# Optimization experiments

Measured on AMD Instinct MI355X. Metric: run time of the kernel, lower is better.

Reference implementation:

```python
import jax, jax.numpy as jnp
import numpy as np
from jax import lax

N_STATES = 128
N_NL = 64
N_IN = 64
N_OUT = 32
N_SYS = 16
FILT = 24
GAMMA = 1e-3
Q_VAL = 10.0
BETA = 1e5
EPS = 1e-3
BATCH = 131072


def setup_inputs() -> dict:
    key = jax.random.key(0)
    ks = jax.random.split(key, 11)
    std = 0.1
    return {
        "inpt": jax.random.normal(ks[0], (BATCH, N_IN), jnp.float32),
        "state": jax.random.normal(ks[1], (BATCH, N_STATES), jnp.float32),
        "X": jax.random.normal(ks[2], (2 * N_STATES + N_NL, 2 * N_STATES + N_NL), jnp.float32) * std,
        "Y1": jax.random.normal(ks[3], (N_STATES, N_STATES), jnp.float32) * std,
        "X3": jax.random.normal(ks[4], (N_OUT, N_OUT), jnp.float32) * std,
        "Y3": jax.random.normal(ks[5], (N_OUT, N_OUT), jnp.float32) * std,
        "Z3": jax.random.normal(ks[6], (abs(N_IN - N_OUT), N_OUT), jnp.float32) * std,
        "B2": jax.random.normal(ks[7], (N_STATES, N_IN), jnp.float32) * std,
        "C2": jax.random.normal(ks[8], (N_OUT, N_STATES), jnp.float32) * std,
        "D21": jax.random.normal(ks[9], (N_OUT, N_NL), jnp.float32) * std,
        "D12": jax.random.normal(ks[10], (N_NL, N_IN), jnp.float32) * std,
    }


def _derived(X, Y1, X3, Y3, Z3, B2, C2, D21, D12):
    # set_model_param(): build contracting REN matrices from free params.
    s = min(N_IN, N_OUT)  # = N_OUT here
    Q = -Q_VAL * jnp.eye(N_OUT, dtype=X.dtype)
    m = N_IN - N_SYS
    R_diag = jnp.concatenate([
        BETA * jnp.ones(N_SYS), GAMMA * jnp.ones(FILT - 1),
        jnp.array([BETA]), GAMMA * jnp.ones(m - FILT)]).astype(X.dtype)
    R = jnp.diag(R_diag)
    I_s = jnp.eye(s, dtype=X.dtype)
    M = X3.T @ X3 + Y3 - Y3.T + Z3.T @ Z3 + EPS * I_s
    Minv = jnp.linalg.inv(I_s + M)
    # n_outputs < n_inputs branch
    N = jnp.concatenate([Minv @ (I_s - M), -2.0 * Minv @ Z3.T], axis=1)  # [n_out, n_in]
    Lq = jnp.linalg.cholesky(-Q).T
    Lr = jnp.linalg.cholesky(R).T
    D22 = jnp.linalg.inv(Lq) @ N @ Lr  # [n_out, n_in]
    R_cal = R + D22.T @ Q @ D22
    R_cal_inv = jnp.linalg.inv(R_cal)
    C2_cal = (D22.T @ Q @ C2).T            # [n_states, n_in]
    D21_cal = (D22.T @ Q @ D21).T - D12    # [n_nl, n_in]
    vec_r = jnp.concatenate([C2_cal, D21_cal, B2], axis=0)
    psi_r = vec_r @ R_cal_inv @ vec_r.T
    vec_q = jnp.concatenate([C2.T, D21.T, jnp.zeros((N_STATES, N_OUT), X.dtype)], axis=0)
    psi_q = vec_q @ Q @ vec_q.T
    n = 2 * N_STATES + N_NL
    H = X.T @ X + EPS * jnp.eye(n, dtype=X.dtype) + psi_r - psi_q
    ns, nl = N_STATES, N_NL
    H11 = H[:ns, :ns]
    H21 = H[ns:ns + nl, :ns]
    H22 = H[ns:ns + nl, ns:ns + nl]
    H31 = H[ns + nl:, :ns]
    H32 = H[ns + nl:, ns:ns + nl]
    H33 = H[ns + nl:, ns + nl:]
    Fm = H31
    B1 = H32
    E = 0.5 * (H11 + H33 + Y1 - Y1.T)
    Lam = 0.5 * jnp.diag(H22)
    D11 = -jnp.tril(H22, k=-1)  # strictly lower triangular
    C1 = -H21
    return Fm, B1, E, Lam, C1, D11, D22


def _ren_forward(inpt, state, X, Y1, X3, Y3, Z3, B2, C2, D21, D12):
    Fm, B1, E, Lam, C1, D11, D22 = _derived(X, Y1, X3, Y3, Z3, B2, C2, D21, D12)
    B = state.shape[0]
    # precompute the state/input contribution to every nonlinearity row
    a = state @ C1.T + inpt @ D12.T  # [B, n_nl] (bias = 0, bias=False)

    def step(w, xs):
        i, a_col, d11_row, lam = xs
        v = a_col + w @ d11_row                 # forward substitution: D11 strictly lower
        w = w.at[:, i].set(jnp.tanh(v / lam))
        return w, None

    w0 = jnp.zeros((B, N_NL), dtype=state.dtype)
    xs = (jnp.arange(N_NL), a.T, D11, Lam)
    w, _ = lax.scan(step, w0, xs)

    E_x_ = state @ Fm.T + w @ B1.T + inpt @ B2.T
    state_plus = E_x_ @ jnp.linalg.inv(E).T
    output = state @ C2.T + w @ D21.T + inpt @ D22.T
    return output, state_plus


def reference(inpt, state, X, Y1, X3, Y3, Z3, B2, C2, D21, D12):
    return _ren_forward(inpt, state, X, Y1, X3, Y3, Z3, B2, C2, D21, D12)
```

## Files before the change

### kernel.cpp

```cpp
#include <hip/hip_runtime.h>
#include <math.h>

#define BATCH 131072
#define NTOT 320

typedef __attribute__((ext_vector_type(8))) short short8;
typedef __attribute__((ext_vector_type(4))) float f32x4;

#define WS_D22   0
#define WS_VR    2048
#define WS_T     22528
#define WS_H     43008
#define WS_E     145408
#define WS_EINV  161792
#define WS_WEXT  178176
#define WS_D11   210944
#define WS_ILAM  215040
#define WS_BFU   215104
#define U_WATH 0
#define U_WATL 16384
#define U_WOT  32768
#define U_WSPH 40960
#define U_WSPL 73728
#define WS_M    (WS_H)
#define WS_A32M (WS_H + 1024)
#define WS_RC   (WS_H + 2048)
#define SC_AI   (WS_H)
#define SC_P    (WS_H + 4096)
#define SC_S    (WS_H + 8192)
#define SC_Q    (WS_H + 12288)
#define SC_R    (WS_H + 16384)

__device__ inline unsigned short f2bf(float x){
    unsigned u = __builtin_bit_cast(unsigned, x);
    u += 0x7FFFu + ((u >> 16) & 1u);
    return (unsigned short)(u >> 16);
}
__device__ inline float bf2f(unsigned short h){
    unsigned u = ((unsigned)h) << 16;
    return __builtin_bit_cast(float, u);
}
__device__ inline float r_diag(int j) {
    return (j < 16 || j == 39) ? 100000.0f : 0.001f;
}

__global__ __launch_bounds__(256) void k_der1a(
    const float* __restrict__ X3, const float* __restrict__ Y3,
    const float* __restrict__ Z3, float* __restrict__ ws)
{
    int idx = blockIdx.x*256 + threadIdx.x;
    if (idx >= 1024) return;
    int i = idx >> 5, j = idx & 31;
    float s = 0.f;
    for (int k = 0; k < 32; ++k)
        s += X3[k*32+i]*X3[k*32+j] + Z3[k*32+i]*Z3[k*32+j];
    s += Y3[i*32+j] - Y3[j*32+i];
    if (i == j) s += 0.001f;
    ws[WS_M + idx]    = s;
    ws[WS_A32M + idx] = s + (i == j ? 1.f : 0.f);
}

__global__ __launch_bounds__(1024) void k_gj32(float* __restrict__ ws)
{
    __shared__ float A32[32*33];
    const int t = threadIdx.x;
    const int i = t >> 5, j = t & 31;
    A32[i*33+j] = ws[WS_A32M + i*32 + j];
    __syncthreads();
    for (int k = 0; k < 32; ++k) {
        float ip = 1.f / A32[k*33+k];
        float f  = A32[i*33+k];
        float pj = A32[k*33+j];
        __syncthreads();
        float nv;
        if (i == k) nv = (j == k) ? ip : pj*ip;
        else        nv = (j == k) ? (-f*ip) : (A32[i*33+j] - f*ip*pj);
        A32[i*33+j] = nv;
        __syncthreads();
    }
    ws[WS_A32M + i*32 + j] = A32[i*33+j];
}

__global__ __launch_bounds__(512) void k_der1b(
    const float* __restrict__ Z3, float* __restrict__ ws)
{
    __shared__ float Ms[1024], Mi[1024], D22s[2048];
    const int t = threadIdx.x;
    for (int idx = t; idx < 1024; idx += 512) {
        Ms[idx] = ws[WS_M + idx];
        Mi[idx] = ws[WS_A32M + idx];
    }
    __syncthreads();
    for (int idx = t; idx < 2048; idx += 512) {
        int i = idx >> 6, j = idx & 63;
        float s = 0.f;
        if (j < 32) {
            for (int k = 0; k < 32; ++k) {
                float im = (k == j ? 1.f : 0.f) - Ms[k*32+j];
                s += Mi[i*32+k]*im;
            }
        } else {
            int jj = j - 32;
            for (int k = 0; k < 32; ++k) s += Mi[i*32+k]*Z3[jj*32+k];
            s *= -2.f;
        }
        float d22 = s * sqrtf(r_diag(j)) * 0.31622776601683794f;
        D22s[idx] = d22;
        ws[WS_D22 + idx] = d22;
    }
    __syncthreads();
    for (int idx = t; idx < 4096; idx += 512) {
        int i = idx >> 6, j = idx & 63;
        float s = 0.f;
        for (int k = 0; k < 32; ++k) s += D22s[k*64+i]*D22s[k*64+j];
        float v = -10.f*s;
        if (i == j) v += r_diag(i);
        ws[WS_RC + idx] = v;
    }
}

__global__ __launch_bounds__(256) void kS_gj64g(float* __restrict__ ws,
    int srcOff, int srcStride, int dstOff, int dstStride)
{
    __shared__ float piv[2][64];
    __shared__ float fcol[2][64];
    __shared__ float ipd[2];
    const int t = threadIdx.x;
    const int q = t >> 6;
    const int i = t & 63;
    const int c0 = q*16;

    float Ar[16];
    {
        const float* Rin = ws + srcOff + i*srcStride + c0;
        #pragma unroll
        for (int jj = 0; jj < 4; ++jj) {
            float4 v = *(const float4*)(Rin + jj*4);
            Ar[jj*4+0]=v.x; Ar[jj*4+1]=v.y; Ar[jj*4+2]=v.z; Ar[jj*4+3]=v.w;
        }
    }

    for (int k = 0; k < 64; ++k) {
        const int b  = k & 1;
        const int kq = k >> 4;
        const int kj = k & 15;

        float f_own = Ar[0];
        #pragma unroll
        for (int jj = 1; jj < 16; ++jj) f_own = (jj == kj) ? Ar[jj] : f_own;

        if (q == kq) fcol[b][i] = f_own;
        if (i == k) {
            #pragma unroll
            for (int jj = 0; jj < 4; ++jj) {
                float4 v;
                v.x = Ar[jj*4+0] + ((q==kq && jj*4+0==kj) ? 1.f : 0.f);
                v.y = Ar[jj*4+1] + ((q==kq && jj*4+1==kj) ? 1.f : 0.f);
                v.z = Ar[jj*4+2] + ((q==kq && jj*4+2==kj) ? 1.f : 0.f);
                v.w = Ar[jj*4+3] + ((q==kq && jj*4+3==kj) ? 1.f : 0.f);
                *(float4*)(&piv[b][c0 + jj*4]) = v;
            }
            if (q == kq) ipd[b] = 1.f / f_own;
        }
        __syncthreads();

        const float ipv = ipd[b];
        if (i == k) {
            #pragma unroll
            for (int jj = 0; jj < 16; ++jj)
                Ar[jj] = (q==kq && jj==kj) ? ipv : Ar[jj]*ipv;
        } else {
            const float g = fcol[b][i] * ipv;
            #pragma unroll
            for (int jj = 0; jj < 4; ++jj) {
                float4 pv = *(const float4*)(&piv[b][c0 + jj*4]);
                Ar[jj*4+0] -= g*pv.x;
                Ar[jj*4+1] -= g*pv.y;
                Ar[jj*4+2] -= g*pv.z;
                Ar[jj*4+3] -= g*pv.w;
            }
        }
    }

    {
        float* Rout = ws + dstOff + i*dstStride + c0;
        #pragma unroll
        for (int jj = 0; jj < 4; ++jj) {
            float4 v;
            v.x=Ar[jj*4+0]; v.y=Ar[jj*4+1]; v.z=Ar[jj*4+2]; v.w=Ar[jj*4+3];
            *(float4*)(Rout + jj*4) = v;
        }
    }
}

__global__ __launch_bounds__(256) void k_vecr(
    const float* __restrict__ B2, const float* __restrict__ C2,
    const float* __restrict__ D21, const float* __restrict__ D12,
    float* __restrict__ ws)
{
    int idx = blockIdx.x*256 + threadIdx.x;
    if (idx >= 320*64) return;
    int i = idx >> 6, j = idx & 63;
    const float* D22 = ws + WS_D22;
    float v;
    if (i < 128) {
        float s = 0.f;
        for (int k = 0; k < 32; ++k) s += C2[k*128+i]*D22[k*64+j];
        v = -10.f*s;
    } else if (i < 192) {
        int ii = i - 128;
        float s = 0.f;
        for (int k = 0; k < 32; ++k) s += D21[k*64+ii]*D22[k*64+j];
        v = -10.f*s - D12[ii*64+j];
    } else {
        v = B2[(i-192)*64 + j];
    }
    ws[WS_VR+idx] = v;
}

__global__ __launch_bounds__(256) void k_T(float* __restrict__ ws)
{
    int idx = blockIdx.x*256 + threadIdx.x;
    if (idx >= 320*64) return;
    int i = idx >> 6, j = idx & 63;
    const float* VR = ws + WS_VR + i*64;
    const float* RC = ws + WS_RC;
    float s = 0.f;
    for (int k = 0; k < 64; ++k) s += VR[k] * RC[k*64+j];
    ws[WS_T+idx] = s;
}

__global__ void k_H(const float* __restrict__ X, const float* __restrict__ C2,
                    const float* __restrict__ D21, float* __restrict__ ws)
{
    int idx = blockIdx.x*256 + threadIdx.x;
    if (idx >= NTOT*NTOT) return;
    int i = idx / NTOT, j = idx % NTOT;
    float s = (i == j) ? 0.001f : 0.f;
    for (int k = 0; k < NTOT; ++k) s += X[k*NTOT+i]*X[k*NTOT+j];
    const float* T  = ws + WS_T;
    const float* vr = ws + WS_VR;
    float s2 = 0.f;
    for (int k = 0; k < 64; ++k) s2 += T[i*64+k]*vr[j*64+k];
    s += s2;
    if (i < 192 && j < 192) {
        float s3 = 0.f;
        for (int k = 0; k < 32; ++k) {
            float qi = (i < 128) ? C2[k*128+i] : D21[k*64 + (i-128)];
            float qj = (j < 128) ? C2[k*128+j] : D21[k*64 + (j-128)];
            s3 += qi*qj;
        }
        s += 10.f*s3;
    }
    ws[WS_H + idx] = s;
}

__global__ void k_extract(const float* __restrict__ Y1, const float* __restrict__ C2,
                          const float* __restrict__ D21, const float* __restrict__ D12,
                          const float* __restrict__ B2, float* __restrict__ ws)
{
    const float* H = ws + WS_H;
    unsigned short* bfb = (unsigned short*)(ws + WS_BFU);
    int tid = blockIdx.x*blockDim.x + threadIdx.x;
    int nth = gridDim.x*blockDim.x;
    for (int idx = tid; idx < 128*128; idx += nth) {
        int i = idx >> 7, j = idx & 127;
        ws[WS_E+idx] = 0.5f*(H[i*320+j] + H[(192+i)*320 + 192+j] + Y1[i*128+j] - Y1[j*128+i]);
    }
    for (int i = tid; i < 64; i += nth)
        ws[WS_ILAM+i] = 2.0f / H[(128+i)*320 + 128+i];
    for (int idx = tid; idx < 64*64; idx += nth) {
        int i = idx >> 6, j = idx & 63;
        ws[WS_D11+idx] = (j < i) ? -H[(128+i)*320 + 128+j] : 0.f;
    }
    for (int idx = tid; idx < 128*256; idx += nth) {
        int m = idx >> 8, k = idx & 255;
        ws[WS_WEXT+idx] = (k < 192) ? H[(192+m)*320 + k] : B2[m*64 + (k-192)];
    }
    for (int idx = tid; idx < 64*256; idx += nth) {
        int j = idx >> 8, k = idx & 255;
        float v;
        if (k < 128)      v = -H[(128+j)*320 + k];
        else if (k < 192) v = 0.f;
        else              v = D12[j*64 + (k-192)];
        unsigned short hi = f2bf(v);
        bfb[U_WATH+idx] = hi;
        bfb[U_WATL+idx] = f2bf(v - bf2f(hi));
    }
    const float* D22 = ws + WS_D22;
    for (int idx = tid; idx < 32*256; idx += nth) {
        int c = idx >> 8, k = idx & 255;
        float v;
        if (k < 128)      v = C2[c*128+k];
        else if (k < 192) v = D21[c*64 + (k-128)];
        else              v = D22[c*64 + (k-192)];
        bfb[U_WOT+idx] = f2bf(v);
    }
}

__global__ __launch_bounds__(256) void kS_P(float* __restrict__ ws)
{
    int idx = blockIdx.x*256 + threadIdx.x;
    int i = idx >> 6, j = idx & 63;
    const float* AI = ws + SC_AI + i*64;
    const float* E  = ws + WS_E;
    float s = 0.f;
    for (int k = 0; k < 64; ++k) s += AI[k] * E[k*128 + 64 + j];
    ws[SC_P + idx] = s;
}
__global__ __launch_bounds__(256) void kS_S(float* __restrict__ ws)
{
    int idx = blockIdx.x*256 + threadIdx.x;
    int i = idx >> 6, j = idx & 63;
    const float* E = ws + WS_E;
    const float* C = E + (64+i)*128;
    const float* P = ws + SC_P;
    float s = E[(64+i)*128 + 64 + j];
    for (int k = 0; k < 64; ++k) s -= C[k] * P[k*64 + j];
    ws[SC_S + idx] = s;
}
__global__ __launch_bounds__(256) void kS_Q(float* __restrict__ ws)
{
    int idx = blockIdx.x*256 + threadIdx.x;
    int i = idx >> 6, j = idx & 63;
    const float* E = ws + WS_E;
    const float* C = E + (64+i)*128;
    const float* AI = ws + SC_AI;
    float s = 0.f;
    for (int k = 0; k < 64; ++k) s += C[k] * AI[k*64 + j];
    ws[SC_Q + idx] = s;
}
__global__ __launch_bounds__(256) void kS_R(float* __restrict__ ws)
{
    int idx = blockIdx.x*256 + threadIdx.x;
    int i = idx >> 6, j = idx & 63;
    const float* Si = ws + SC_S + i*64;
    const float* Q  = ws + SC_Q;
    float s = 0.f;
    for (int k = 0; k < 64; ++k) s += Si[k] * Q[k*64 + j];
    ws[SC_R + idx] = s;
    ws[WS_EINV + (64+i)*128 + j] = -s;
}
__global__ __launch_bounds__(256) void kS_TL(float* __restrict__ ws)
{
    int idx = blockIdx.x*256 + threadIdx.x;
    int i = idx >> 6, j = idx & 63;
    const float* P  = ws + SC_P + i*64;
    const float* R2 = ws + SC_R;
    const float* Si = ws + SC_S;
    float s1 = ws[SC_AI + idx];
    float s2 = 0.f;
    for (int k = 0; k < 64; ++k) {
        s1 += P[k] * R2[k*64 + j];
        s2 += P[k] * Si[k*64 + j];
    }
    ws[WS_EINV + i*128 + j]        = s1;
    ws[WS_EINV + i*128 + 64 + j]   = -s2;
    ws[WS_EINV + (64+i)*128 + 64 + j] = Si[i*64 + j];
}

__global__ __launch_bounds__(256) void k_Wsp(float* __restrict__ ws)
{
    int i = blockIdx.x;
    int k = threadIdx.x;
    const float* Einv = ws + WS_EINV + i*128;
    const float* WexT = ws + WS_WEXT;
    unsigned short* bfb = (unsigned short*)(ws + WS_BFU);
    float s = 0.f;
    for (int m = 0; m < 128; ++m) s += Einv[m] * WexT[m*256 + k];
    unsigned short hi = f2bf(s);
    bfb[U_WSPH + i*256 + k] = hi;
    bfb[U_WSPL + i*256 + k] = f2bf(s - bf2f(hi));
}

__global__ __launch_bounds__(256, 4) void k_batch(
    const float* __restrict__ inpt, const float* __restrict__ state,
    const float* __restrict__ ws, float* __restrict__ out)
{
    __shared__ unsigned short zsh[64*256];
    __shared__ unsigned short D11t[64*64];
    const int t = threadIdx.x;
    const int row0 = blockIdx.x * 64;
    const unsigned short* bfb = (const unsigned short*)(ws + WS_BFU);

    for (int idx = t; idx < 64*16; idx += 256) {
        int r = idx >> 4, c = idx & 15;
        const float4* p = (const float4*)(state + (size_t)(row0+r)*128 + c*8);
        float4 f0 = p[0], f1 = p[1];
        short8 h;
        h[0]=(short)f2bf(f0.x); h[1]=(short)f2bf(f0.y); h[2]=(short)f2bf(f0.z); h[3]=(short)f2bf(f0.w);
        h[4]=(short)f2bf(f1.x); h[5]=(short)f2bf(f1.y); h[6]=(short)f2bf(f1.z); h[7]=(short)f2bf(f1.w);
        *(short8*)(&zsh[r*256 + ((c ^ (r&7)) << 3)]) = h;
    }
    for (int idx = t; idx < 64*8; idx += 256) {
        int r = idx >> 3, cl = idx & 7, c = 24 + cl;
        const float4* p = (const float4*)(inpt + (size_t)(row0+r)*64 + cl*8);
        float4 f0 = p[0], f1 = p[1];
        short8 h;
        h[0]=(short)f2bf(f0.x); h[1]=(short)f2bf(f0.y); h[2]=(short)f2bf(f0.z); h[3]=(short)f2bf(f0.w);
        h[4]=(short)f2bf(f1.x); h[5]=(short)f2bf(f1.y); h[6]=(short)f2bf(f1.z); h[7]=(short)f2bf(f1.w);
        *(short8*)(&zsh[r*256 + ((c ^ (r&7)) << 3)]) = h;
    }
    for (int idx = t; idx < 4096; idx += 256) {
        int j = idx >> 6, i = idx & 63;
        float v = (i == j) ? ws[WS_ILAM + j] : ws[WS_D11 + i*64 + j];
        D11t[idx] = f2bf(v);
    }
    __syncthreads();

    const int wv = t >> 6, lane = t & 63, lr = lane & 15, lk = lane >> 4;

    {
        const unsigned short* WATH = bfb + U_WATH;
        const unsigned short* WATL = bfb + U_WATL;
        f32x4 acc1[4] = {};
        const int ks1[6] = {0,1,2,3,6,7};
        #pragma unroll
        for (int s = 0; s < 6; ++s) {
            int ks = ks1[s];
            short8 bh = *(const short8*)(&WATH[(wv*16+lr)*256 + ks*32 + lk*8]);
            short8 bl = *(const short8*)(&WATL[(wv*16+lr)*256 + ks*32 + lk*8]);
            #pragma unroll
            for (int rt = 0; rt < 4; ++rt) {
                int row = rt*16 + lr, c = ks*4 + lk;
                short8 a = *(const short8*)(&zsh[row*256 + ((c ^ (row&7)) << 3)]);
                acc1[rt] = __builtin_amdgcn_mfma_f32_16x16x32_bf16(a, bh, acc1[rt], 0, 0, 0);
                acc1[rt] = __builtin_amdgcn_mfma_f32_16x16x32_bf16(a, bl, acc1[rt], 0, 0, 0);
            }
        }
        __syncthreads();
        const int ac = wv*16 + lr;
        const int cch = 16 + (ac >> 3), coff = ac & 7;
        #pragma unroll
        for (int rt = 0; rt < 4; ++rt)
            #pragma unroll
            for (int r = 0; r < 4; ++r) {
                int row = rt*16 + lk*4 + r;
                zsh[row*256 + ((cch ^ (row&7)) << 3) + coff] = f2bf(acc1[rt][r]);
            }
    }
    __syncthreads();

    {
        const int r  = wv*16 + (lane >> 2);
        const int qq = lane & 3;
        float acc[16];
        #pragma unroll
        for (int s = 0; s < 16; ++s) {
            int i = qq*16 + s;
            int cch = 16 + (i >> 3);
            acc[s] = bf2f(zsh[r*256 + ((cch ^ (r&7)) << 3) + (i & 7)]);
        }
        float wloc[16];
        #pragma unroll
        for (int j = 0; j < 64; ++j) {
            float diag = bf2f(D11t[j*64 + j]);
            float v = acc[j & 15];
            float x = v * diag;
            float e = __expf(2.f*x);
            float wc = 1.f - __fdividef(2.f, e + 1.f);
            int src = (lane & 0x3C) | (j >> 4);
            float wj = __shfl(wc, src, 64);
            if ((j >> 4) == qq) wloc[j & 15] = wj;
            #pragma unroll
            for (int s = 0; s < 16; ++s)
                acc[s] += wj * bf2f(D11t[j*64 + qq*16 + s]);
        }
        #pragma unroll
        for (int cc = 0; cc < 2; ++cc) {
            int ch = 16 + qq*2 + cc;
            short8 h;
            #pragma unroll
            for (int e2 = 0; e2 < 8; ++e2) h[e2] = (short)f2bf(wloc[cc*8 + e2]);
            *(short8*)(&zsh[r*256 + ((ch ^ (r&7)) << 3)]) = h;
        }
    }
    __syncthreads();

    {
        const unsigned short* WOT  = bfb + U_WOT;
        const unsigned short* WSPH = bfb + U_WSPH;
        const unsigned short* WSPL = bfb + U_WSPL;
        f32x4 acc[3][4] = {};
        const int nt = (wv < 2) ? 3 : 2;
        #pragma unroll
        for (int ks = 0; ks < 8; ++ks) {
            short8 afr[4];
            #pragma unroll
            for (int rt = 0; rt < 4; ++rt) {
                int row = rt*16 + lr, c = ks*4 + lk;
                afr[rt] = *(const short8*)(&zsh[row*256 + ((c ^ (row&7)) << 3)]);
            }
            #pragma unroll
            for (int tt = 0; tt < 3; ++tt) {
                if (tt < nt) {
                    int ct = wv + tt*4;
                    if (ct < 2) {
                        short8 b = *(const short8*)(&WOT[(ct*16+lr)*256 + ks*32 + lk*8]);
                        #pragma unroll
                        for (int rt = 0; rt < 4; ++rt)
                            acc[tt][rt] = __builtin_amdgcn_mfma_f32_16x16x32_bf16(afr[rt], b, acc[tt][rt], 0, 0, 0);
                    } else {
                        short8 bh = *(const short8*)(&WSPH[((ct-2)*16+lr)*256 + ks*32 + lk*8]);
                        short8 bl = *(const short8*)(&WSPL[((ct-2)*16+lr)*256 + ks*32 + lk*8]);
                        #pragma unroll
                        for (int rt = 0; rt < 4; ++rt) {
                            acc[tt][rt] = __builtin_amdgcn_mfma_f32_16x16x32_bf16(afr[rt], bh, acc[tt][rt], 0, 0, 0);
                            acc[tt][rt] = __builtin_amdgcn_mfma_f32_16x16x32_bf16(afr[rt], bl, acc[tt][rt], 0, 0, 0);
                        }
                    }
                }
            }
        }
        float* sp = out + (size_t)BATCH*32;
        #pragma unroll
        for (int tt = 0; tt < 3; ++tt) {
            if (tt < nt) {
                int ct = wv + tt*4;
                #pragma unroll
                for (int rt = 0; rt < 4; ++rt) {
                    int rowb = row0 + rt*16 + lk*4;
                    #pragma unroll
                    for (int r = 0; r < 4; ++r) {
                        float vv = acc[tt][rt][r];
                        if (ct < 2) out[(size_t)(rowb+r)*32  + ct*16 + lr]     = vv;
                        else        sp[(size_t)(rowb+r)*128 + (ct-2)*16 + lr] = vv;
                    }
                }
            }
        }
    }
}

extern "C" void kernel_launch(void* const* d_in, const int* in_sizes, int n_in,
                              void* d_out, int out_size, void* d_ws, size_t ws_size,
                              hipStream_t stream)
{
    const float* inpt  = (const float*)d_in[0];
    const float* state = (const float*)d_in[1];
    const float* X   = (const float*)d_in[2];
    const float* Y1  = (const float*)d_in[3];
    const float* X3  = (const float*)d_in[4];
    const float* Y3  = (const float*)d_in[5];
    const float* Z3  = (const float*)d_in[6];
    const float* B2  = (const float*)d_in[7];
    const float* C2  = (const float*)d_in[8];
    const float* D21 = (const float*)d_in[9];
    const float* D12 = (const float*)d_in[10];
    float* ws  = (float*)d_ws;
    float* out = (float*)d_out;

    k_der1a<<<4, 256, 0, stream>>>(X3, Y3, Z3, ws);
    k_gj32<<<1, 1024, 0, stream>>>(ws);
    k_der1b<<<1, 512, 0, stream>>>(Z3, ws);
    kS_gj64g<<<1, 256, 0, stream>>>(ws, WS_RC, 64, WS_RC, 64);
    k_vecr<<<80, 256, 0, stream>>>(B2, C2, D21, D12, ws);
    k_T<<<80, 256, 0, stream>>>(ws);
    k_H<<<(NTOT*NTOT + 255)/256, 256, 0, stream>>>(X, C2, D21, ws);
    k_extract<<<128, 256, 0, stream>>>(Y1, C2, D21, D12, B2, ws);
    kS_gj64g<<<1, 256, 0, stream>>>(ws, WS_E, 128, SC_AI, 64);
    kS_P<<<16, 256, 0, stream>>>(ws);
    kS_S<<<16, 256, 0, stream>>>(ws);
    kS_gj64g<<<1, 256, 0, stream>>>(ws, SC_S, 64, SC_S, 64);
    kS_Q<<<16, 256, 0, stream>>>(ws);
    kS_R<<<16, 256, 0, stream>>>(ws);
    kS_TL<<<16, 256, 0, stream>>>(ws);
    k_Wsp<<<128, 256, 0, stream>>>(ws);
    k_batch<<<BATCH/64, 256, 0, stream>>>(inpt, state, ws, out);
}
```

Baseline: 299.3 us.

## Fuse small setup kernels and halve batch tile rows for more parallel recurrence

Merges the three 32x32 derivation kernels into one single-block kernel and folds the Q product into the P kernel, cutting the number of serial launches. The batch kernel now processes 32 rows per block instead of 64, so the sequential tanh forward-substitution spreads over 8 lanes per row with 8 accumulators each, and occupancy is raised to 6 blocks. This shortens the per-thread serial chain and lowers register pressure. In exchange it doubles the grid, shuffles more often, and reloads weight fragments for fewer rows per block.

```diff
diff --git a/kernel.cpp b/kernel.cpp
--- a/kernel.cpp
+++ b/kernel.cpp
@@ -22,8 +22,6 @@
 #define U_WOT  32768
 #define U_WSPH 40960
 #define U_WSPL 73728
-#define WS_M    (WS_H)
-#define WS_A32M (WS_H + 1024)
 #define WS_RC   (WS_H + 2048)
 #define SC_AI   (WS_H)
 #define SC_P    (WS_H + 4096)
@@ -44,28 +42,24 @@
     return (j < 16 || j == 39) ? 100000.0f : 0.001f;
 }
 
-__global__ __launch_bounds__(256) void k_der1a(
+__global__ __launch_bounds__(1024) void kF_abc(
     const float* __restrict__ X3, const float* __restrict__ Y3,
     const float* __restrict__ Z3, float* __restrict__ ws)
 {
-    int idx = blockIdx.x*256 + threadIdx.x;
-    if (idx >= 1024) return;
-    int i = idx >> 5, j = idx & 31;
-    float s = 0.f;
-    for (int k = 0; k < 32; ++k)
-        s += X3[k*32+i]*X3[k*32+j] + Z3[k*32+i]*Z3[k*32+j];
-    s += Y3[i*32+j] - Y3[j*32+i];
-    if (i == j) s += 0.001f;
-    ws[WS_M + idx]    = s;
-    ws[WS_A32M + idx] = s + (i == j ? 1.f : 0.f);
-}
-
-__global__ __launch_bounds__(1024) void k_gj32(float* __restrict__ ws)
-{
+    __shared__ float Msh[32*33];
     __shared__ float A32[32*33];
+    __shared__ float D22s[2048];
     const int t = threadIdx.x;
     const int i = t >> 5, j = t & 31;
-    A32[i*33+j] = ws[WS_A32M + i*32 + j];
+    {
+        float s = 0.f;
+        for (int k = 0; k < 32; ++k)
+            s += X3[k*32+i]*X3[k*32+j] + Z3[k*32+i]*Z3[k*32+j];
+        s += Y3[i*32+j] - Y3[j*32+i];
+        if (i == j) s += 0.001f;
+        Msh[i*33+j] = s;
+        A32[i*33+j] = s + (i == j ? 1.f : 0.f);
+    }
     __syncthreads();
     for (int k = 0; k < 32; ++k) {
         float ip = 1.f / A32[k*33+k];
@@ -78,43 +72,30 @@
         A32[i*33+j] = nv;
         __syncthreads();
     }
-    ws[WS_A32M + i*32 + j] = A32[i*33+j];
-}
-
-__global__ __launch_bounds__(512) void k_der1b(
-    const float* __restrict__ Z3, float* __restrict__ ws)
-{
-    __shared__ float Ms[1024], Mi[1024], D22s[2048];
-    const int t = threadIdx.x;
-    for (int idx = t; idx < 1024; idx += 512) {
-        Ms[idx] = ws[WS_M + idx];
-        Mi[idx] = ws[WS_A32M + idx];
-    }
-    __syncthreads();
-    for (int idx = t; idx < 2048; idx += 512) {
-        int i = idx >> 6, j = idx & 63;
-        float s = 0.f;
-        if (j < 32) {
+    for (int idx = t; idx < 2048; idx += 1024) {
+        int i2 = idx >> 6, j2 = idx & 63;
+        float s = 0.f;
+        if (j2 < 32) {
             for (int k = 0; k < 32; ++k) {
-                float im = (k == j ? 1.f : 0.f) - Ms[k*32+j];
-                s += Mi[i*32+k]*im;
+                float im = (k == j2 ? 1.f : 0.f) - Msh[k*33+j2];
+                s += A32[i2*33+k]*im;
             }
         } else {
-            int jj = j - 32;
-            for (int k = 0; k < 32; ++k) s += Mi[i*32+k]*Z3[jj*32+k];
+            int jj = j2 - 32;
+            for (int k = 0; k < 32; ++k) s += A32[i2*33+k]*Z3[jj*32+k];
             s *= -2.f;
         }
-        float d22 = s * sqrtf(r_diag(j)) * 0.31622776601683794f;
+        float d22 = s * sqrtf(r_diag(j2)) * 0.31622776601683794f;
         D22s[idx] = d22;
         ws[WS_D22 + idx] = d22;
     }
     __syncthreads();
-    for (int idx = t; idx < 4096; idx += 512) {
-        int i = idx >> 6, j = idx & 63;
-        float s = 0.f;
-        for (int k = 0; k < 32; ++k) s += D22s[k*64+i]*D22s[k*64+j];
+    for (int idx = t; idx < 4096; idx += 1024) {
+        int i2 = idx >> 6, j2 = idx & 63;
+        float s = 0.f;
+        for (int k = 0; k < 32; ++k) s += D22s[k*64+i2]*D22s[k*64+j2];
         float v = -10.f*s;
-        if (i == j) v += r_diag(i);
+        if (i2 == j2) v += r_diag(i2);
         ws[WS_RC + idx] = v;
     }
 }
@@ -139,16 +120,13 @@
             Ar[jj*4+0]=v.x; Ar[jj*4+1]=v.y; Ar[jj*4+2]=v.z; Ar[jj*4+3]=v.w;
         }
     }
-
     for (int k = 0; k < 64; ++k) {
         const int b  = k & 1;
         const int kq = k >> 4;
         const int kj = k & 15;
-
         float f_own = Ar[0];
         #pragma unroll
         for (int jj = 1; jj < 16; ++jj) f_own = (jj == kj) ? Ar[jj] : f_own;
-
         if (q == kq) fcol[b][i] = f_own;
         if (i == k) {
             #pragma unroll
@@ -163,7 +141,6 @@
             if (q == kq) ipd[b] = 1.f / f_own;
         }
         __syncthreads();
-
         const float ipv = ipd[b];
         if (i == k) {
             #pragma unroll
@@ -181,7 +158,6 @@
             }
         }
     }
-
     {
         float* Rout = ws + dstOff + i*dstStride + c0;
         #pragma unroll
@@ -298,15 +274,25 @@
     }
 }
 
-__global__ __launch_bounds__(256) void kS_P(float* __restrict__ ws)
-{
-    int idx = blockIdx.x*256 + threadIdx.x;
-    int i = idx >> 6, j = idx & 63;
-    const float* AI = ws + SC_AI + i*64;
+__global__ __launch_bounds__(256) void kS_PQ(float* __restrict__ ws)
+{
+    int gid = blockIdx.x*256 + threadIdx.x;
     const float* E  = ws + WS_E;
-    float s = 0.f;
-    for (int k = 0; k < 64; ++k) s += AI[k] * E[k*128 + 64 + j];
-    ws[SC_P + idx] = s;
+    if (gid < 4096) {
+        int i = gid >> 6, j = gid & 63;
+        const float* AI = ws + SC_AI + i*64;
+        float s = 0.f;
+        for (int k = 0; k < 64; ++k) s += AI[k] * E[k*128 + 64 + j];
+        ws[SC_P + gid] = s;
+    } else {
+        int idx = gid - 4096;
+        int i = idx >> 6, j = idx & 63;
+        const float* C = E + (64+i)*128;
+        const float* AI = ws + SC_AI;
+        float s = 0.f;
+        for (int k = 0; k < 64; ++k) s += C[k] * AI[k*64 + j];
+        ws[SC_Q + idx] = s;
+    }
 }
 __global__ __launch_bounds__(256) void kS_S(float* __restrict__ ws)
 {
@@ -318,17 +304,6 @@
     float s = E[(64+i)*128 + 64 + j];
     for (int k = 0; k < 64; ++k) s -= C[k] * P[k*64 + j];
     ws[SC_S + idx] = s;
-}
-__global__ __launch_bounds__(256) void kS_Q(float* __restrict__ ws)
-{
-    int idx = blockIdx.x*256 + threadIdx.x;
-    int i = idx >> 6, j = idx & 63;
-    const float* E = ws + WS_E;
-    const float* C = E + (64+i)*128;
-    const float* AI = ws + SC_AI;
-    float s = 0.f;
-    for (int k = 0; k < 64; ++k) s += C[k] * AI[k*64 + j];
-    ws[SC_Q + idx] = s;
 }
 __global__ __launch_bounds__(256) void kS_R(float* __restrict__ ws)
 {
@@ -354,8 +329,8 @@
         s1 += P[k] * R2[k*64 + j];
         s2 += P[k] * Si[k*64 + j];
     }
-    ws[WS_EINV + i*128 + j]        = s1;
-    ws[WS_EINV + i*128 + 64 + j]   = -s2;
+    ws[WS_EINV + i*128 + j]           = s1;
+    ws[WS_EINV + i*128 + 64 + j]      = -s2;
     ws[WS_EINV + (64+i)*128 + 64 + j] = Si[i*64 + j];
 }
 
@@ -373,17 +348,18 @@
     bfb[U_WSPL + i*256 + k] = f2bf(s - bf2f(hi));
 }
 
-__global__ __launch_bounds__(256, 4) void k_batch(
+#define ROWS 32
+__global__ __launch_bounds__(256, 6) void k_batch(
     const float* __restrict__ inpt, const float* __restrict__ state,
     const float* __restrict__ ws, float* __restrict__ out)
 {
-    __shared__ unsigned short zsh[64*256];
+    __shared__ unsigned short zsh[ROWS*256];
     __shared__ unsigned short D11t[64*64];
     const int t = threadIdx.x;
-    const int row0 = blockIdx.x * 64;
+    const int row0 = blockIdx.x * ROWS;
     const unsigned short* bfb = (const unsigned short*)(ws + WS_BFU);
 
-    for (int idx = t; idx < 64*16; idx += 256) {
+    for (int idx = t; idx < ROWS*16; idx += 256) {
         int r = idx >> 4, c = idx & 15;
         const float4* p = (const float4*)(state + (size_t)(row0+r)*128 + c*8);
         float4 f0 = p[0], f1 = p[1];
@@ -392,7 +368,7 @@
         h[4]=(short)f2bf(f1.x); h[5]=(short)f2bf(f1.y); h[6]=(short)f2bf(f1.z); h[7]=(short)f2bf(f1.w);
         *(short8*)(&zsh[r*256 + ((c ^ (r&7)) << 3)]) = h;
     }
-    for (int idx = t; idx < 64*8; idx += 256) {
+    for (int idx = t; idx < ROWS*8; idx += 256) {
         int r = idx >> 3, cl = idx & 7, c = 24 + cl;
         const float4* p = (const float4*)(inpt + (size_t)(row0+r)*64 + cl*8);
         float4 f0 = p[0], f1 = p[1];
@@ -413,7 +389,7 @@
     {
         const unsigned short* WATH = bfb + U_WATH;
         const unsigned short* WATL = bfb + U_WATL;
-        f32x4 acc1[4] = {};
+        f32x4 acc1[2] = {};
         const int ks1[6] = {0,1,2,3,6,7};
         #pragma unroll
         for (int s = 0; s < 6; ++s) {
@@ -421,7 +397,7 @@
             short8 bh = *(const short8*)(&WATH[(wv*16+lr)*256 + ks*32 + lk*8]);
             short8 bl = *(const short8*)(&WATL[(wv*16+lr)*256 + ks*32 + lk*8]);
             #pragma unroll
-            for (int rt = 0; rt < 4; ++rt) {
+            for (int rt = 0; rt < 2; ++rt) {
                 int row = rt*16 + lr, c = ks*4 + lk;
                 short8 a = *(const short8*)(&zsh[row*256 + ((c ^ (row&7)) << 3)]);
                 acc1[rt] = __builtin_amdgcn_mfma_f32_16x16x32_bf16(a, bh, acc1[rt], 0, 0, 0);
@@ -432,7 +408,7 @@
         const int ac = wv*16 + lr;
         const int cch = 16 + (ac >> 3), coff = ac & 7;
         #pragma unroll
-        for (int rt = 0; rt < 4; ++rt)
+        for (int rt = 0; rt < 2; ++rt)
             #pragma unroll
             for (int r = 0; r < 4; ++r) {
                 int row = rt*16 + lk*4 + r;
@@ -442,37 +418,34 @@
     __syncthreads();
 
     {
-        const int r  = wv*16 + (lane >> 2);
-        const int qq = lane & 3;
-        float acc[16];
-        #pragma unroll
-        for (int s = 0; s < 16; ++s) {
-            int i = qq*16 + s;
-            int cch = 16 + (i >> 3);
-            acc[s] = bf2f(zsh[r*256 + ((cch ^ (r&7)) << 3) + (i & 7)]);
-        }
-        float wloc[16];
+        const int r  = wv*8 + (lane >> 3);
+        const int qq = lane & 7;
+        float acc[8];
+        {
+            short8 av = *(const short8*)(&zsh[r*256 + (((16+qq) ^ (r&7)) << 3)]);
+            #pragma unroll
+            for (int s = 0; s < 8; ++s) acc[s] = bf2f((unsigned short)av[s]);
+        }
+        float wloc[8];
         #pragma unroll
         for (int j = 0; j < 64; ++j) {
             float diag = bf2f(D11t[j*64 + j]);
-            float v = acc[j & 15];
+            float v = acc[j & 7];
             float x = v * diag;
             float e = __expf(2.f*x);
             float wc = 1.f - __fdividef(2.f, e + 1.f);
-            int src = (lane & 0x3C) | (j >> 4);
+            int src = (lane & 0x38) | (j >> 3);
             float wj = __shfl(wc, src, 64);
-            if ((j >> 4) == qq) wloc[j & 15] = wj;
-            #pragma unroll
-            for (int s = 0; s < 16; ++s)
-                acc[s] += wj * bf2f(D11t[j*64 + qq*16 + s]);
-        }
-        #pragma unroll
-        for (int cc = 0; cc < 2; ++cc) {
-            int ch = 16 + qq*2 + cc;
+            if ((j >> 3) == qq) wloc[j & 7] = wj;
+            #pragma unroll
+            for (int s = 0; s < 8; ++s)
+                acc[s] += wj * bf2f(D11t[j*64 + qq*8 + s]);
+        }
+        {
             short8 h;
             #pragma unroll
-            for (int e2 = 0; e2 < 8; ++e2) h[e2] = (short)f2bf(wloc[cc*8 + e2]);
-            *(short8*)(&zsh[r*256 + ((ch ^ (r&7)) << 3)]) = h;
+            for (int e2 = 0; e2 < 8; ++e2) h[e2] = (short)f2bf(wloc[e2]);
+            *(short8*)(&zsh[r*256 + (((16+qq) ^ (r&7)) << 3)]) = h;
         }
     }
     __syncthreads();
@@ -481,13 +454,13 @@
         const unsigned short* WOT  = bfb + U_WOT;
         const unsigned short* WSPH = bfb + U_WSPH;
         const unsigned short* WSPL = bfb + U_WSPL;
-        f32x4 acc[3][4] = {};
+        f32x4 acc[3][2] = {};
         const int nt = (wv < 2) ? 3 : 2;
         #pragma unroll
         for (int ks = 0; ks < 8; ++ks) {
-            short8 afr[4];
-            #pragma unroll
-            for (int rt = 0; rt < 4; ++rt) {
+            short8 afr[2];
+            #pragma unroll
+            for (int rt = 0; rt < 2; ++rt) {
                 int row = rt*16 + lr, c = ks*4 + lk;
                 afr[rt] = *(const short8*)(&zsh[row*256 + ((c ^ (row&7)) << 3)]);
             }
@@ -498,13 +471,13 @@
                     if (ct < 2) {
                         short8 b = *(const short8*)(&WOT[(ct*16+lr)*256 + ks*32 + lk*8]);
                         #pragma unroll
-                        for (int rt = 0; rt < 4; ++rt)
+                        for (int rt = 0; rt < 2; ++rt)
                             acc[tt][rt] = __builtin_amdgcn_mfma_f32_16x16x32_bf16(afr[rt], b, acc[tt][rt], 0, 0, 0);
                     } else {
                         short8 bh = *(const short8*)(&WSPH[((ct-2)*16+lr)*256 + ks*32 + lk*8]);
                         short8 bl = *(const short8*)(&WSPL[((ct-2)*16+lr)*256 + ks*32 + lk*8]);
                         #pragma unroll
-                        for (int rt = 0; rt < 4; ++rt) {
+                        for (int rt = 0; rt < 2; ++rt) {
                             acc[tt][rt] = __builtin_amdgcn_mfma_f32_16x16x32_bf16(afr[rt], bh, acc[tt][rt], 0, 0, 0);
                             acc[tt][rt] = __builtin_amdgcn_mfma_f32_16x16x32_bf16(afr[rt], bl, acc[tt][rt], 0, 0, 0);
                         }
@@ -518,7 +491,7 @@
             if (tt < nt) {
                 int ct = wv + tt*4;
                 #pragma unroll
-                for (int rt = 0; rt < 4; ++rt) {
+                for (int rt = 0; rt < 2; ++rt) {
                     int rowb = row0 + rt*16 + lk*4;
                     #pragma unroll
                     for (int r = 0; r < 4; ++r) {
@@ -550,21 +523,18 @@
     float* ws  = (float*)d_ws;
     float* out = (float*)d_out;
 
-    k_der1a<<<4, 256, 0, stream>>>(X3, Y3, Z3, ws);
-    k_gj32<<<1, 1024, 0, stream>>>(ws);
-    k_der1b<<<1, 512, 0, stream>>>(Z3, ws);
+    kF_abc<<<1, 1024, 0, stream>>>(X3, Y3, Z3, ws);
     kS_gj64g<<<1, 256, 0, stream>>>(ws, WS_RC, 64, WS_RC, 64);
     k_vecr<<<80, 256, 0, stream>>>(B2, C2, D21, D12, ws);
     k_T<<<80, 256, 0, stream>>>(ws);
     k_H<<<(NTOT*NTOT + 255)/256, 256, 0, stream>>>(X, C2, D21, ws);
     k_extract<<<128, 256, 0, stream>>>(Y1, C2, D21, D12, B2, ws);
     kS_gj64g<<<1, 256, 0, stream>>>(ws, WS_E, 128, SC_AI, 64);
-    kS_P<<<16, 256, 0, stream>>>(ws);
+    kS_PQ<<<32, 256, 0, stream>>>(ws);
     kS_S<<<16, 256, 0, stream>>>(ws);
     kS_gj64g<<<1, 256, 0, stream>>>(ws, SC_S, 64, SC_S, 64);
-    kS_Q<<<16, 256, 0, stream>>>(ws);
     kS_R<<<16, 256, 0, stream>>>(ws);
     kS_TL<<<16, 256, 0, stream>>>(ws);
     k_Wsp<<<128, 256, 0, stream>>>(ws);
-    k_batch<<<BATCH/64, 256, 0, stream>>>(inpt, state, ws, out);
-}
+    k_batch<<<BATCH/ROWS, 256, 0, stream>>>(inpt, state, ws, out);
+}
```

Measured after the change: 333.6 us. +11.4%, slower.
